# Kernel optimization log

Hardware: AMD Instinct MI355X
Metric: run time of the kernel (lower is better)

## Reference

```python
import jax, jax.numpy as jnp
import numpy as np

INPUT_DIM = 64
AUG_DIM = 64
HIDDEN = 256
BATCH = 4096
T = 50


def setup_inputs() -> dict:
    key = jax.random.key(0)
    k0, k1, k2 = jax.random.split(key, 3)
    D = INPUT_DIM + AUG_DIM
    x0 = jax.random.normal(k0, (BATCH, INPUT_DIM), jnp.float32)
    t = jnp.linspace(0.0, 1.0, T).astype(jnp.float32)
    W1 = jax.random.normal(k1, (D, HIDDEN), jnp.float32) / np.sqrt(D).astype(np.float32)
    b1 = jnp.zeros((HIDDEN,), jnp.float32)
    W2 = jax.random.normal(k2, (HIDDEN, D), jnp.float32) / np.sqrt(HIDDEN).astype(np.float32)
    b2 = jnp.zeros((D,), jnp.float32)
    return {"x0": x0, "t": t, "W1": W1, "b1": b1, "W2": W2, "b2": b2}


def reference(x0, t, W1, b1, W2, b2):
    # ode_func: time-independent MLP on the augmented state [B, D]
    def f(ti, y):
        return jnp.tanh(y @ W1 + b1) @ W2 + b2

    B = x0.shape[0]
    # augment with zeros -> [B, INPUT_DIM + AUG_DIM]
    y0 = jnp.concatenate([x0, jnp.zeros((B, AUG_DIM), x0.dtype)], axis=-1)

    # torchdiffeq 'rk4' fixed-grid solver: one 3/8-rule RK4 step per interval
    def step(y, ts):
        t0, t1 = ts
        dt = t1 - t0
        third = dt * (1.0 / 3.0)
        k1 = f(t0, y)
        k2 = f(t0 + third, y + third * k1)
        k3 = f(t0 + 2.0 * third, y + dt * (k2 - k1 * (1.0 / 3.0)))
        k4 = f(t1, y + dt * (k1 - k2 + k3))
        y1 = y + dt * 0.125 * (k1 + 3.0 * (k2 + k3) + k4)
        return y1, y1

    _, ys = jax.lax.scan(step, y0, (t[:-1], t[1:]))  # [T-1, B, D]
    sol = jnp.concatenate([y0[None], ys], axis=0)    # [T, B, D]
    return sol[..., :INPUT_DIM]                      # drop augmented dims
```

## Files before the change

kernel.cpp:

```cpp
#include <hip/hip_runtime.h>

typedef __attribute__((ext_vector_type(8))) _Float16 f16x8;
typedef __attribute__((ext_vector_type(4))) _Float16 f16x4;
typedef __attribute__((ext_vector_type(2))) _Float16 f16x2;
typedef __attribute__((ext_vector_type(4))) float f32x4;
typedef __attribute__((ext_vector_type(2))) float f32x2;

#define T_STEPS 49
#define BM 16
#define OUTSTRIDE (4096*64)
#define YSTR 132
#define HSTR 260

__device__ __forceinline__ f16x8 ld_frag(const _Float16* p) {
  f16x4 a = *(const f16x4*)p;
  f16x4 b = *(const f16x4*)(p + 4);
  return __builtin_shufflevector(a, b, 0,1,2,3,4,5,6,7);
}
__device__ __forceinline__ float vsub(float a, float b) {
  float r;
  asm("v_sub_f32 %0, %1, %2" : "=v"(r) : "v"(a), "v"(b));
  return r;
}
__device__ __forceinline__ f32x2 vfma2(f32x2 a, f32x2 b, f32x2 c) {
  return __builtin_elementwise_fma(a, b, c);
}
__device__ __forceinline__ f32x2 tanh2(f32x2 x) {
  const f32x2 c2  = { 2.885390081777927f, 2.885390081777927f };
  const f32x2 one = { 1.f, 1.f };
  const f32x2 m2  = { -2.f, -2.f };
  f32x2 t = x * c2;
  f32x2 e;
  e[0] = __builtin_amdgcn_exp2f(t[0]);
  e[1] = __builtin_amdgcn_exp2f(t[1]);
  f32x2 ep1 = e + one;
  f32x2 r;
  r[0] = __builtin_amdgcn_rcpf(ep1[0]);
  r[1] = __builtin_amdgcn_rcpf(ep1[1]);
  return vfma2(r, m2, one);
}
__device__ __forceinline__ f16x4 cvt4(f32x2 a, f32x2 b) {
  f16x2 h0 = __builtin_bit_cast(f16x2, __builtin_amdgcn_cvt_pkrtz(a[0], a[1]));
  f16x2 h1 = __builtin_bit_cast(f16x2, __builtin_amdgcn_cvt_pkrtz(b[0], b[1]));
  return __builtin_shufflevector(h0, h1, 0,1,2,3);
}

__global__ __launch_bounds__(512)
void node_rk4_kernel(const float* __restrict__ x0, const float* __restrict__ tarr,
                     const float* __restrict__ W1, const float* __restrict__ b1,
                     const float* __restrict__ W2, const float* __restrict__ b2,
                     float* __restrict__ out)
{
  __shared__ __align__(16) _Float16 Yh[16][YSTR];
  __shared__ __align__(16) _Float16 Hh[16][HSTR];

  const int tid  = threadIdx.x;
  const int w    = tid >> 6;
  const int lane = tid & 63;
  const int m    = lane & 15;
  const int g    = lane >> 4;
  const int row0 = (int)blockIdx.x * BM;

  f16x8 wB1[2][4], wB2[8];
#pragma unroll
  for (int c = 0; c < 2; ++c)
#pragma unroll
    for (int kk = 0; kk < 4; ++kk) {
      f16x8 v;
#pragma unroll
      for (int j = 0; j < 8; ++j)
        v[j] = (_Float16)W1[(kk*32 + 8*g + j)*256 + (32*w + 16*c + m)];
      wB1[c][kk] = v;
    }
#pragma unroll
  for (int kk = 0; kk < 8; ++kk) {
    f16x8 v;
#pragma unroll
    for (int j = 0; j < 8; ++j)
      v[j] = (_Float16)W2[(kk*32 + 8*g + j)*128 + (16*w + m)];
    wB2[kk] = v;
  }
  f32x4 bb1[2], bb2v;
#pragma unroll
  for (int c = 0; c < 2; ++c)
#pragma unroll
    for (int i = 0; i < 4; ++i) bb1[c][i] = b1[16*(2*w + c) + 4*g + i];
#pragma unroll
  for (int i = 0; i < 4; ++i) bb2v[i] = b2[16*w + 4*g + i];

  const int ccol = 16*w + 4*g;
  f32x2 y[2], k1[2], k2[2], k3[2], yn[2];
  if (ccol < 64) {
    const float4 v = *(const float4*)&x0[(row0 + m)*64 + ccol];
    y[0][0]=v.x; y[0][1]=v.y; y[1][0]=v.z; y[1][1]=v.w;
  } else {
    y[0] = (f32x2){0.f,0.f}; y[1] = (f32x2){0.f,0.f};
  }
  yn[0] = y[0]; yn[1] = y[1];
  if (ccol < 64) {
    float4 v; v.x=y[0][0]; v.y=y[0][1]; v.z=y[1][0]; v.w=y[1][1];
    *(float4*)&out[(row0 + m)*64 + ccol] = v;
  }
  *(f16x4*)&Yh[m][ccol] = cvt4(yn[0], yn[1]);
  __syncthreads();

  for (int step = 0; step < T_STEPS; ++step) {
    const float dt = vsub(tarr[step+1], tarr[step]);
    const f32x2 dt2      = { dt, dt };
    const f32x2 third2   = { dt*(1.f/3.f), dt*(1.f/3.f) };
    const f32x2 mthird2  = { -1.f/3.f, -1.f/3.f };
    const f32x2 three2   = { 3.f, 3.f };
    const f32x2 dt8      = { dt*0.125f, dt*0.125f };

#pragma unroll
    for (int stage = 0; stage < 4; ++stage) {
      f32x4 acc0 = bb1[0], acc1 = bb1[1];
#pragma unroll
      for (int kk = 0; kk < 4; ++kk) {
        f16x8 a = ld_frag(&Yh[m][kk*32 + 8*g]);
        acc0 = __builtin_amdgcn_mfma_f32_16x16x32_f16(wB1[0][kk], a, acc0, 0,0,0);
        acc1 = __builtin_amdgcn_mfma_f32_16x16x32_f16(wB1[1][kk], a, acc1, 0,0,0);
      }
      {
        f32x2 t00 = tanh2((f32x2){acc0[0], acc0[1]});
        f32x2 t01 = tanh2((f32x2){acc0[2], acc0[3]});
        f32x2 t10 = tanh2((f32x2){acc1[0], acc1[1]});
        f32x2 t11 = tanh2((f32x2){acc1[2], acc1[3]});
        *(f16x4*)&Hh[m][16*(2*w+0) + 4*g] = cvt4(t00, t01);
        *(f16x4*)&Hh[m][16*(2*w+1) + 4*g] = cvt4(t10, t11);
      }
      __syncthreads();

      f32x4 accA = bb2v;
      f32x4 accB = { 0.f, 0.f, 0.f, 0.f };
#pragma unroll
      for (int kk = 0; kk < 4; ++kk) {
        f16x8 aA = ld_frag(&Hh[m][kk*32 + 8*g]);
        f16x8 aB = ld_frag(&Hh[m][(kk+4)*32 + 8*g]);
        accA = __builtin_amdgcn_mfma_f32_16x16x32_f16(wB2[kk],   aA, accA, 0,0,0);
        accB = __builtin_amdgcn_mfma_f32_16x16x32_f16(wB2[kk+4], aB, accB, 0,0,0);
      }
      f32x2 ks[2];
      ks[0] = (f32x2){accA[0],accA[1]} + (f32x2){accB[0],accB[1]};
      ks[1] = (f32x2){accA[2],accA[3]} + (f32x2){accB[2],accB[3]};

      if (stage == 0) {
#pragma unroll
        for (int p = 0; p < 2; ++p) { k1[p] = ks[p]; yn[p] = vfma2(k1[p], third2, y[p]); }
      } else if (stage == 1) {
#pragma unroll
        for (int p = 0; p < 2; ++p) {
          k2[p] = ks[p];
          f32x2 a = vfma2(k1[p], mthird2, k2[p]);
          yn[p] = vfma2(a, dt2, y[p]);
        }
      } else if (stage == 2) {
#pragma unroll
        for (int p = 0; p < 2; ++p) {
          k3[p] = ks[p];
          f32x2 b = (k1[p] - k2[p]) + k3[p];
          yn[p] = vfma2(b, dt2, y[p]);
        }
      } else {
#pragma unroll
        for (int p = 0; p < 2; ++p) {
          f32x2 s1 = k2[p] + k3[p];
          f32x2 s2 = vfma2(s1, three2, k1[p]);
          f32x2 s3 = s2 + ks[p];
          y[p] = vfma2(s3, dt8, y[p]);
          yn[p] = y[p];
        }
        if (ccol < 64) {
          float4 v; v.x=y[0][0]; v.y=y[0][1]; v.z=y[1][0]; v.w=y[1][1];
          *(float4*)&out[(size_t)(step+1)*OUTSTRIDE + (row0 + m)*64 + ccol] = v;
        }
      }
      *(f16x4*)&Yh[m][ccol] = cvt4(yn[0], yn[1]);
      __syncthreads();
    }
  }
}

extern "C" void kernel_launch(void* const* d_in, const int* in_sizes, int n_in,
                              void* d_out, int out_size, void* d_ws, size_t ws_size,
                              hipStream_t stream) {
  const float* x0 = (const float*)d_in[0];
  const float* t  = (const float*)d_in[1];
  const float* W1 = (const float*)d_in[2];
  const float* b1 = (const float*)d_in[3];
  const float* W2 = (const float*)d_in[4];
  const float* b2 = (const float*)d_in[5];
  float* out = (float*)d_out;
  hipLaunchKernelGGL(node_rk4_kernel, dim3(4096/BM), dim3(512), 0, stream,
                     x0, t, W1, b1, W2, b2, out);
}
```

Baseline: 150.1 us.

## Specialize warps into layer-1 and layer-2 groups with doubled per-warp tiles

Splits the eight waves into two groups: waves 4-7 compute the first layer (64 hidden columns each) and waves 0-3 compute the second layer and the RK4 update (32 state columns each), instead of every wave doing both layers. Each wave now keeps only one weight matrix slice in registers and issues more independent MFMAs per pass. It also widens the LDS row padding to change bank mapping. The cost is that half the waves sit idle at each barrier-separated phase, since the two layers still run one after the other.

```diff
diff --git a/kernel.cpp b/kernel.cpp
--- a/kernel.cpp
+++ b/kernel.cpp
@@ -9,8 +9,8 @@
 #define T_STEPS 49
 #define BM 16
 #define OUTSTRIDE (4096*64)
-#define YSTR 132
-#define HSTR 260
+#define YSTR 140
+#define HSTR 268
 
 __device__ __forceinline__ f16x8 ld_frag(const _Float16* p) {
   f16x4 a = *(const f16x4*)p;
@@ -60,48 +60,62 @@
   const int m    = lane & 15;
   const int g    = lane >> 4;
   const int row0 = (int)blockIdx.x * BM;
-
-  f16x8 wB1[2][4], wB2[8];
-#pragma unroll
-  for (int c = 0; c < 2; ++c)
-#pragma unroll
-    for (int kk = 0; kk < 4; ++kk) {
-      f16x8 v;
-#pragma unroll
-      for (int j = 0; j < 8; ++j)
-        v[j] = (_Float16)W1[(kk*32 + 8*g + j)*256 + (32*w + 16*c + m)];
-      wB1[c][kk] = v;
+  const bool isA = (w < 4);
+  const int wb   = w - 4;
+
+  f16x8 wB[16];
+  f32x4 bias[4];
+  if (isA) {
+#pragma unroll
+    for (int t = 0; t < 2; ++t)
+#pragma unroll
+      for (int kk = 0; kk < 8; ++kk) {
+        f16x8 v;
+#pragma unroll
+        for (int j = 0; j < 8; ++j)
+          v[j] = (_Float16)W2[(kk*32 + 8*g + j)*128 + (32*w + 16*t + m)];
+        wB[t*8 + kk] = v;
+      }
+#pragma unroll
+    for (int t = 0; t < 2; ++t)
+#pragma unroll
+      for (int i = 0; i < 4; ++i) bias[t][i] = b2[32*w + 16*t + 4*g + i];
+  } else {
+#pragma unroll
+    for (int c = 0; c < 4; ++c)
+#pragma unroll
+      for (int kk = 0; kk < 4; ++kk) {
+        f16x8 v;
+#pragma unroll
+        for (int j = 0; j < 8; ++j)
+          v[j] = (_Float16)W1[(kk*32 + 8*g + j)*256 + (64*wb + 16*c + m)];
+        wB[c*4 + kk] = v;
+      }
+#pragma unroll
+    for (int c = 0; c < 4; ++c)
+#pragma unroll
+      for (int i = 0; i < 4; ++i) bias[c][i] = b1[64*wb + 16*c + 4*g + i];
+  }
+
+  f32x2 y[2][2], k1[2][2], k2[2][2], k3[2][2], yn[2][2];
+#pragma unroll
+  for (int t = 0; t < 2; ++t)
+#pragma unroll
+    for (int p = 0; p < 2; ++p) { y[t][p] = (f32x2){0.f,0.f}; yn[t][p] = y[t][p]; }
+  if (isA) {
+    if (w < 2) {
+#pragma unroll
+      for (int t = 0; t < 2; ++t) {
+        const float4 v = *(const float4*)&x0[(row0 + m)*64 + 32*w + 16*t + 4*g];
+        y[t][0] = (f32x2){v.x, v.y}; y[t][1] = (f32x2){v.z, v.w};
+        yn[t][0] = y[t][0]; yn[t][1] = y[t][1];
+        *(float4*)&out[(row0 + m)*64 + 32*w + 16*t + 4*g] = v;
+      }
     }
 #pragma unroll
-  for (int kk = 0; kk < 8; ++kk) {
-    f16x8 v;
-#pragma unroll
-    for (int j = 0; j < 8; ++j)
-      v[j] = (_Float16)W2[(kk*32 + 8*g + j)*128 + (16*w + m)];
-    wB2[kk] = v;
+    for (int t = 0; t < 2; ++t)
+      *(f16x4*)&Yh[m][32*w + 16*t + 4*g] = cvt4(yn[t][0], yn[t][1]);
   }
-  f32x4 bb1[2], bb2v;
-#pragma unroll
-  for (int c = 0; c < 2; ++c)
-#pragma unroll
-    for (int i = 0; i < 4; ++i) bb1[c][i] = b1[16*(2*w + c) + 4*g + i];
-#pragma unroll
-  for (int i = 0; i < 4; ++i) bb2v[i] = b2[16*w + 4*g + i];
-
-  const int ccol = 16*w + 4*g;
-  f32x2 y[2], k1[2], k2[2], k3[2], yn[2];
-  if (ccol < 64) {
-    const float4 v = *(const float4*)&x0[(row0 + m)*64 + ccol];
-    y[0][0]=v.x; y[0][1]=v.y; y[1][0]=v.z; y[1][1]=v.w;
-  } else {
-    y[0] = (f32x2){0.f,0.f}; y[1] = (f32x2){0.f,0.f};
-  }
-  yn[0] = y[0]; yn[1] = y[1];
-  if (ccol < 64) {
-    float4 v; v.x=y[0][0]; v.y=y[0][1]; v.z=y[1][0]; v.w=y[1][1];
-    *(float4*)&out[(row0 + m)*64 + ccol] = v;
-  }
-  *(f16x4*)&Yh[m][ccol] = cvt4(yn[0], yn[1]);
   __syncthreads();
 
   for (int step = 0; step < T_STEPS; ++step) {
@@ -114,68 +128,89 @@
 
 #pragma unroll
     for (int stage = 0; stage < 4; ++stage) {
-      f32x4 acc0 = bb1[0], acc1 = bb1[1];
-#pragma unroll
-      for (int kk = 0; kk < 4; ++kk) {
-        f16x8 a = ld_frag(&Yh[m][kk*32 + 8*g]);
-        acc0 = __builtin_amdgcn_mfma_f32_16x16x32_f16(wB1[0][kk], a, acc0, 0,0,0);
-        acc1 = __builtin_amdgcn_mfma_f32_16x16x32_f16(wB1[1][kk], a, acc1, 0,0,0);
-      }
-      {
-        f32x2 t00 = tanh2((f32x2){acc0[0], acc0[1]});
-        f32x2 t01 = tanh2((f32x2){acc0[2], acc0[3]});
-        f32x2 t10 = tanh2((f32x2){acc1[0], acc1[1]});
-        f32x2 t11 = tanh2((f32x2){acc1[2], acc1[3]});
-        *(f16x4*)&Hh[m][16*(2*w+0) + 4*g] = cvt4(t00, t01);
-        *(f16x4*)&Hh[m][16*(2*w+1) + 4*g] = cvt4(t10, t11);
+      if (!isA) {
+        f32x4 acc[4];
+#pragma unroll
+        for (int c = 0; c < 4; ++c) acc[c] = bias[c];
+#pragma unroll
+        for (int kk = 0; kk < 4; ++kk) {
+          f16x8 a = ld_frag(&Yh[m][kk*32 + 8*g]);
+#pragma unroll
+          for (int c = 0; c < 4; ++c)
+            acc[c] = __builtin_amdgcn_mfma_f32_16x16x32_f16(wB[c*4 + kk], a, acc[c], 0,0,0);
+        }
+#pragma unroll
+        for (int c = 0; c < 4; ++c) {
+          f32x2 t0 = tanh2((f32x2){acc[c][0], acc[c][1]});
+          f32x2 t1 = tanh2((f32x2){acc[c][2], acc[c][3]});
+          *(f16x4*)&Hh[m][64*wb + 16*c + 4*g] = cvt4(t0, t1);
+        }
       }
       __syncthreads();
 
-      f32x4 accA = bb2v;
-      f32x4 accB = { 0.f, 0.f, 0.f, 0.f };
-#pragma unroll
-      for (int kk = 0; kk < 4; ++kk) {
-        f16x8 aA = ld_frag(&Hh[m][kk*32 + 8*g]);
-        f16x8 aB = ld_frag(&Hh[m][(kk+4)*32 + 8*g]);
-        accA = __builtin_amdgcn_mfma_f32_16x16x32_f16(wB2[kk],   aA, accA, 0,0,0);
-        accB = __builtin_amdgcn_mfma_f32_16x16x32_f16(wB2[kk+4], aB, accB, 0,0,0);
-      }
-      f32x2 ks[2];
-      ks[0] = (f32x2){accA[0],accA[1]} + (f32x2){accB[0],accB[1]};
-      ks[1] = (f32x2){accA[2],accA[3]} + (f32x2){accB[2],accB[3]};
-
-      if (stage == 0) {
-#pragma unroll
-        for (int p = 0; p < 2; ++p) { k1[p] = ks[p]; yn[p] = vfma2(k1[p], third2, y[p]); }
-      } else if (stage == 1) {
-#pragma unroll
-        for (int p = 0; p < 2; ++p) {
-          k2[p] = ks[p];
-          f32x2 a = vfma2(k1[p], mthird2, k2[p]);
-          yn[p] = vfma2(a, dt2, y[p]);
-        }
-      } else if (stage == 2) {
-#pragma unroll
-        for (int p = 0; p < 2; ++p) {
-          k3[p] = ks[p];
-          f32x2 b = (k1[p] - k2[p]) + k3[p];
-          yn[p] = vfma2(b, dt2, y[p]);
-        }
-      } else {
-#pragma unroll
-        for (int p = 0; p < 2; ++p) {
-          f32x2 s1 = k2[p] + k3[p];
-          f32x2 s2 = vfma2(s1, three2, k1[p]);
-          f32x2 s3 = s2 + ks[p];
-          y[p] = vfma2(s3, dt8, y[p]);
-          yn[p] = y[p];
-        }
-        if (ccol < 64) {
-          float4 v; v.x=y[0][0]; v.y=y[0][1]; v.z=y[1][0]; v.w=y[1][1];
-          *(float4*)&out[(size_t)(step+1)*OUTSTRIDE + (row0 + m)*64 + ccol] = v;
-        }
-      }
-      *(f16x4*)&Yh[m][ccol] = cvt4(yn[0], yn[1]);
+      if (isA) {
+        f32x4 acc[2];
+#pragma unroll
+        for (int t = 0; t < 2; ++t) acc[t] = bias[t];
+#pragma unroll
+        for (int kk = 0; kk < 8; ++kk) {
+          f16x8 a = ld_frag(&Hh[m][kk*32 + 8*g]);
+#pragma unroll
+          for (int t = 0; t < 2; ++t)
+            acc[t] = __builtin_amdgcn_mfma_f32_16x16x32_f16(wB[t*8 + kk], a, acc[t], 0,0,0);
+        }
+        f32x2 ks[2][2];
+#pragma unroll
+        for (int t = 0; t < 2; ++t) {
+          ks[t][0] = (f32x2){acc[t][0], acc[t][1]};
+          ks[t][1] = (f32x2){acc[t][2], acc[t][3]};
+        }
+        if (stage == 0) {
+#pragma unroll
+          for (int t = 0; t < 2; ++t)
+#pragma unroll
+            for (int p = 0; p < 2; ++p) { k1[t][p] = ks[t][p]; yn[t][p] = vfma2(k1[t][p], third2, y[t][p]); }
+        } else if (stage == 1) {
+#pragma unroll
+          for (int t = 0; t < 2; ++t)
+#pragma unroll
+            for (int p = 0; p < 2; ++p) {
+              k2[t][p] = ks[t][p];
+              f32x2 a = vfma2(k1[t][p], mthird2, k2[t][p]);
+              yn[t][p] = vfma2(a, dt2, y[t][p]);
+            }
+        } else if (stage == 2) {
+#pragma unroll
+          for (int t = 0; t < 2; ++t)
+#pragma unroll
+            for (int p = 0; p < 2; ++p) {
+              k3[t][p] = ks[t][p];
+              f32x2 b = (k1[t][p] - k2[t][p]) + k3[t][p];
+              yn[t][p] = vfma2(b, dt2, y[t][p]);
+            }
+        } else {
+#pragma unroll
+          for (int t = 0; t < 2; ++t)
+#pragma unroll
+            for (int p = 0; p < 2; ++p) {
+              f32x2 s1 = k2[t][p] + k3[t][p];
+              f32x2 s2 = vfma2(s1, three2, k1[t][p]);
+              f32x2 s3 = s2 + ks[t][p];
+              y[t][p] = vfma2(s3, dt8, y[t][p]);
+              yn[t][p] = y[t][p];
+            }
+          if (w < 2) {
+#pragma unroll
+            for (int t = 0; t < 2; ++t) {
+              float4 v; v.x=y[t][0][0]; v.y=y[t][0][1]; v.z=y[t][1][0]; v.w=y[t][1][1];
+              *(float4*)&out[(size_t)(step+1)*OUTSTRIDE + (row0 + m)*64 + 32*w + 16*t + 4*g] = v;
+            }
+          }
+        }
+#pragma unroll
+        for (int t = 0; t < 2; ++t)
+          *(f16x4*)&Yh[m][32*w + 16*t + 4*g] = cvt4(yn[t][0], yn[t][1]);
+      }
       __syncthreads();
     }
   }
```

Measured after the change: 156.6 us. 4.3% more time.
